# Optimization experiments

Measured on AMD Instinct MI355X. Metric: run time of the kernel, lower is better.

## Reference

```python
import jax, jax.numpy as jnp
import numpy as np

NS, NI, NC, C, E, M = 50000, 20000, 1000, 128, 1000000, 250000


def setup_inputs() -> dict:
    key = jax.random.key(0)
    ks = jax.random.split(key, 12)
    xavier = (2.0 / (C + C)) ** 0.5  # xavier_normal_ std for square weight
    return {
        "stu_x": jax.random.normal(ks[0], (NS, C), jnp.float32),
        "item_x": jax.random.normal(ks[1], (NI, C), jnp.float32),
        "conc_x": jax.random.normal(ks[2], (NC, C), jnp.float32),
        "W_stu": jax.random.normal(ks[3], (C, C), jnp.float32) * xavier,
        "b_stu": jnp.zeros((C,), jnp.float32),
        "W_item": jax.random.normal(ks[4], (C, C), jnp.float32) * xavier,
        "b_item": jnp.zeros((C,), jnp.float32),
        "W_pred": jax.random.normal(ks[5], (1, C), jnp.float32) * ((2.0 / (1 + C)) ** 0.5),
        "b_pred": jnp.zeros((1,), jnp.float32),
        "stu_track": jax.random.randint(ks[6], (E,), 0, NS, jnp.int32),
        "item_index": jax.random.randint(ks[7], (E,), 0, NI, jnp.int32),
        "conc_index": jax.random.randint(ks[8], (E,), 0, NC, jnp.int32),
        "mean_index": jax.random.randint(ks[9], (E,), 0, M, jnp.int32),
        "num_segments": M,
    }


def _segment_mean(vals, seg_ids, num_segments):
    sums = jax.ops.segment_sum(vals, seg_ids, num_segments=num_segments)
    cnt = jax.ops.segment_sum(jnp.ones((vals.shape[0], 1), vals.dtype), seg_ids,
                              num_segments=num_segments)
    return sums / jnp.maximum(cnt, 1.0)


def reference(stu_x, item_x, conc_x, W_stu, b_stu, W_item, b_item, W_pred, b_pred,
              stu_track, item_index, conc_index, mean_index, num_segments):
    # Feature (stu): shared lin_l=lin_r; aggregate is identity -> per-edge output
    conc_s = conc_x @ W_stu.T          # [NC, C] projected source (concepts)
    stu_p = stu_x @ W_stu.T            # [NS, C] projected target (students)
    stu_feature = jax.nn.sigmoid(conc_s[conc_index] + stu_p[stu_track] + b_stu)  # [E, C]

    # Feature (item): SparseTensor(row=item, col=conc) -> x_j from conc, x_i from item
    conc_i = conc_x @ W_item.T         # [NC, C]
    item_p = item_x @ W_item.T         # [NI, C]
    item_feature = jax.nn.sigmoid(conc_i[conc_index] + item_p[item_index] + b_item)  # [E, C]

    # scatter-mean of per-edge difference over mean_index groups
    pred_input = _segment_mean(stu_feature - item_feature, mean_index, num_segments)  # [M, C]
    pred = jax.nn.sigmoid(pred_input @ W_pred.T + b_pred)  # [M, 1]
    return pred.reshape(-1)
```

## Files before the change

### kernel.cpp

```cpp
#include <hip/hip_runtime.h>

typedef unsigned short u16;
typedef unsigned int   u32;

typedef short short8 __attribute__((ext_vector_type(8)));
typedef float floatx4 __attribute__((ext_vector_type(4)));

#define CDIM 128
#define K_NEG_LOG2E -1.4426950408889634f
#define CNT_SCALE 16777216.0

__device__ __forceinline__ float bf2f_lo(u32 h) {
    union { u32 u; float f; } v; v.u = h << 16; return v.f;
}
__device__ __forceinline__ float bf2f_hi(u32 h) {
    union { u32 u; float f; } v; v.u = h & 0xffff0000u; return v.f;
}
__device__ __forceinline__ u16 f2bf(float f) {
    union { float f; u32 u; } v; v.f = f;
    u32 u = v.u;
    return (u16)((u + 0x7FFFu + ((u >> 16) & 1u)) >> 16);
}
__device__ __forceinline__ float sig_std(float x) {
    return __builtin_amdgcn_rcpf(1.0f + __builtin_amdgcn_exp2f(x * K_NEG_LOG2E));
}

__device__ __forceinline__ float rowsum16(float v) {
    int x;
    x = __builtin_amdgcn_update_dpp(0, __float_as_int(v), 0x111, 0xF, 0xF, true);
    v += __int_as_float(x);
    x = __builtin_amdgcn_update_dpp(0, __float_as_int(v), 0x112, 0xF, 0xF, true);
    v += __int_as_float(x);
    x = __builtin_amdgcn_update_dpp(0, __float_as_int(v), 0x114, 0xF, 0xF, true);
    v += __int_as_float(x);
    x = __builtin_amdgcn_update_dpp(0, __float_as_int(v), 0x118, 0xF, 0xF, true);
    v += __int_as_float(x);
    return v;
}

__global__ __launch_bounds__(256) void prep_kernel(
    const float* __restrict__ Wstu, const float* __restrict__ Witem,
    u32* __restrict__ Wbf_pair, float4* __restrict__ zero4, int nZero4,
    const int* __restrict__ stu_track, const int* __restrict__ item_index,
    const int* __restrict__ conc_index, const int* __restrict__ mean_index,
    int4* __restrict__ idx4, int E)
{
    const int tid = blockIdx.x * blockDim.x + threadIdx.x;
    const int stride = gridDim.x * blockDim.x;
    for (int i = tid; i < 16384; i += stride) {
        const float* W = (i & 8192) ? (Witem - 16384) : Wstu;
        const int j = i * 2;
        u32 lo = f2bf(W[j]     * K_NEG_LOG2E);
        u32 hi = f2bf(W[j + 1] * K_NEG_LOG2E);
        Wbf_pair[i] = lo | (hi << 16);
    }
    const float4 z = {0.f, 0.f, 0.f, 0.f};
    for (int i = tid; i < nZero4; i += stride) zero4[i] = z;
    for (int e = tid; e < E; e += stride) {
        int4 t;
        t.x = stu_track[e]  << 8;
        t.y = item_index[e] << 8;
        t.z = conc_index[e] << 9;
        t.w = mean_index[e] << 3;
        idx4[e] = t;
    }
}

__device__ __forceinline__ void proj_tile16(
    const float* __restrict__ X, const u16* __restrict__ Wbf,
    const float* __restrict__ bias, u16* __restrict__ out,
    int nrows, int ostride, int ooff, int row0, int lane)
{
    const int m = lane & 15;
    const int g = lane >> 4;

    short8 a[4];
    {
        int arow = row0 + m;
        if (arow >= nrows) arow = nrows - 1;
        const float* xrow = X + (size_t)arow * CDIM;
#pragma unroll
        for (int s = 0; s < 4; ++s) {
            float4 f0 = *(const float4*)(xrow + s * 32 + g * 8);
            float4 f1 = *(const float4*)(xrow + s * 32 + g * 8 + 4);
            a[s][0] = (short)f2bf(f0.x); a[s][1] = (short)f2bf(f0.y);
            a[s][2] = (short)f2bf(f0.z); a[s][3] = (short)f2bf(f0.w);
            a[s][4] = (short)f2bf(f1.x); a[s][5] = (short)f2bf(f1.y);
            a[s][6] = (short)f2bf(f1.z); a[s][7] = (short)f2bf(f1.w);
        }
    }

#pragma unroll
    for (int ct = 0; ct < 8; ++ct) {
        const u16* wrow = Wbf + (size_t)(ct * 16 + m) * CDIM;
        floatx4 acc = {0.f, 0.f, 0.f, 0.f};
#pragma unroll
        for (int s = 0; s < 4; ++s) {
            short8 b = *(const short8*)(wrow + s * 32 + g * 8);
            acc = __builtin_amdgcn_mfma_f32_16x16x32_bf16(a[s], b, acc, 0, 0, 0);
        }
        const int col = ct * 16 + m;
        const float badd = bias ? bias[col] * K_NEG_LOG2E : 0.f;
#pragma unroll
        for (int i = 0; i < 4; ++i) {
            int r = row0 + g * 4 + i;
            if (r < nrows)
                out[(size_t)r * ostride + ooff + col] =
                    f2bf(__builtin_amdgcn_exp2f(acc[i] + badd));
        }
    }
}

__global__ __launch_bounds__(256) void proj4_kernel(
    const float* __restrict__ stu_x, const float* __restrict__ item_x,
    const float* __restrict__ conc_x,
    const u16* __restrict__ Wstu_bf, const u16* __restrict__ Witem_bf,
    const float* __restrict__ b_stu, const float* __restrict__ b_item,
    u16* __restrict__ stu_p, u16* __restrict__ item_p, u16* __restrict__ conc_cat,
    int NS, int NI, int NC)
{
    const int lane = threadIdx.x & 63;
    int w = blockIdx.x * 4 + (threadIdx.x >> 6);
    const int T0 = (NS + 15) / 16, T1 = (NI + 15) / 16, T2 = (NC + 15) / 16;

    if (w < T0) { proj_tile16(stu_x, Wstu_bf, nullptr, stu_p, NS, 128, 0, w * 16, lane); return; }
    w -= T0;
    if (w < T1) { proj_tile16(item_x, Witem_bf, nullptr, item_p, NI, 128, 0, w * 16, lane); return; }
    w -= T1;
    if (w < T2) { proj_tile16(conc_x, Wstu_bf, b_stu, conc_cat, NC, 256, 0, w * 16, lane); return; }
    w -= T2;
    if (w < T2) { proj_tile16(conc_x, Witem_bf, b_item, conc_cat, NC, 256, 128, w * 16, lane); return; }
}

__global__ __launch_bounds__(256) void edge_kernel(
    const u16* __restrict__ stu_p, const u16* __restrict__ item_p,
    const u16* __restrict__ conc_cat,
    const int4* __restrict__ idx4,
    const float* __restrict__ w_pred,
    double* __restrict__ sc, int E)
{
    const int lane = threadIdx.x & 63;
    const int sub  = lane & 15;
    const int g    = lane >> 4;
    const int waveId = (int)((blockIdx.x * blockDim.x + threadIdx.x) >> 6);
    const int S      = (int)((gridDim.x * blockDim.x) >> 6);

    const float4 wA = ((const float4*)w_pred)[sub * 2];
    const float4 wB = ((const float4*)w_pred)[sub * 2 + 1];
    float2 w2[4];
    w2[0] = make_float2(wA.x, wA.y); w2[1] = make_float2(wA.z, wA.w);
    w2[2] = make_float2(wB.x, wB.y); w2[3] = make_float2(wB.z, wB.w);
    const u32 lane_off = (u32)sub * 16;

    const int nQuads = (E + 3) >> 2;
    int q = waveId;
    if (q >= nQuads) return;

    auto ldidx = [&](int qq) -> int4 {
        int e = qq * 4 + g;
        e = (e < E) ? e : (E - 1);
        return idx4[e];
    };
    auto compute = [&](const uint4& sv, const uint4& iv,
                       const uint4& ca, const uint4& cb,
                       const int4& I, int qq) {
        const u32 su[4] = {sv.x, sv.y, sv.z, sv.w};
        const u32 iu[4] = {iv.x, iv.y, iv.z, iv.w};
        const u32 au[4] = {ca.x, ca.y, ca.z, ca.w};
        const u32 bu[4] = {cb.x, cb.y, cb.z, cb.w};
        float2 vacc = make_float2(0.f, 0.f);
#pragma unroll
        for (int j = 0; j < 4; ++j) {
            float2 A  = make_float2(bf2f_lo(au[j]), bf2f_hi(au[j]));
            float2 Sx = make_float2(bf2f_lo(su[j]), bf2f_hi(su[j]));
            float2 B  = make_float2(bf2f_lo(bu[j]), bf2f_hi(bu[j]));
            float2 Ix = make_float2(bf2f_lo(iu[j]), bf2f_hi(iu[j]));
            float2 ea = A * Sx;
            float2 eb = B * Ix;
            float2 u  = make_float2(eb.x + 1.f, eb.y + 1.f);
            float2 den = make_float2(fmaf(ea.x, u.x, u.x),
                                     fmaf(ea.y, u.y, u.y));
            float2 num = eb - ea;
            float2 rd = make_float2(__builtin_amdgcn_rcpf(den.x),
                                    __builtin_amdgcn_rcpf(den.y));
            float2 t  = make_float2(num.x * rd.x, num.y * rd.y);
            vacc.x = fmaf(t.x, w2[j].x, vacc.x);
            vacc.y = fmaf(t.y, w2[j].y, vacc.y);
        }
        float v = rowsum16(vacc.x + vacc.y);
        if (sub == 15 && (qq * 4 + g) < E)
            atomicAdd((double*)((char*)sc + (u32)I.w), (double)v + CNT_SCALE);
    };

#define GATH(I_, sv_, iv_, ca_, cb_) { \
        sv_ = *(const uint4*)((const char*)stu_p  + ((u32)(I_).x + lane_off)); \
        iv_ = *(const uint4*)((const char*)item_p + ((u32)(I_).y + lane_off)); \
        const char* cp_ = (const char*)conc_cat + ((u32)(I_).z + lane_off); \
        ca_ = *(const uint4*)cp_; cb_ = *(const uint4*)(cp_ + 256); }

#define STEP(DA, DB, IA, IB, IC) { \
        GATH(I##IB, sv##DB, iv##DB, ca##DB, cb##DB); \
        I##IC = ldidx(q + 2 * S); \
        __builtin_amdgcn_sched_barrier(0); \
        compute(sv##DA, iv##DA, ca##DA, cb##DA, I##IA, q); \
        q += S; \
        if (q >= nQuads) break; }

    int4 I0 = ldidx(q), I1 = ldidx(q + S), I2, I3;
    uint4 sv0, iv0, ca0, cb0, sv1, iv1, ca1, cb1;
    GATH(I0, sv0, iv0, ca0, cb0);

    for (;;) {
        STEP(0, 1, 0, 1, 2)
        STEP(1, 0, 1, 2, 3)
        STEP(0, 1, 2, 3, 0)
        STEP(1, 0, 3, 0, 1)
    }
#undef STEP
#undef GATH
}

__global__ __launch_bounds__(256) void final_kernel(
    const double* __restrict__ sc,
    const float* __restrict__ b_pred, float* __restrict__ out, int M)
{
    const int i = blockIdx.x * blockDim.x + threadIdx.x;
    if (i < M) {
        const double acc = sc[i];
        const double cnt = rint(acc * (1.0 / CNT_SCALE));
        const double sum = acc - cnt * CNT_SCALE;
        const float mean = (float)(sum / fmax(cnt, 1.0));
        out[i] = sig_std(mean + b_pred[0]);
    }
}

extern "C" void kernel_launch(void* const* d_in, const int* in_sizes, int n_in,
                              void* d_out, int out_size, void* d_ws, size_t ws_size,
                              hipStream_t stream) {
    const float* stu_x    = (const float*)d_in[0];
    const float* item_x   = (const float*)d_in[1];
    const float* conc_x   = (const float*)d_in[2];
    const float* W_stu    = (const float*)d_in[3];
    const float* b_stu    = (const float*)d_in[4];
    const float* W_item   = (const float*)d_in[5];
    const float* b_item   = (const float*)d_in[6];
    const float* W_pred   = (const float*)d_in[7];
    const float* b_pred   = (const float*)d_in[8];
    const int* stu_track  = (const int*)d_in[9];
    const int* item_index = (const int*)d_in[10];
    const int* conc_index = (const int*)d_in[11];
    const int* mean_index = (const int*)d_in[12];

    const int NS = in_sizes[0] / CDIM;
    const int NI = in_sizes[1] / CDIM;
    const int NC = in_sizes[2] / CDIM;
    const int E  = in_sizes[9];
    const int M  = out_size;

    double* sc     = (double*)d_ws;
    u16* Wstu_bf   = (u16*)(sc + M);
    u16* Witem_bf  = Wstu_bf + CDIM * CDIM;
    u16* stu_p     = Witem_bf + CDIM * CDIM;
    u16* item_p    = stu_p  + (size_t)NS * CDIM;
    u16* conc_cat  = item_p + (size_t)NI * CDIM;
    int4* idx4     = (int4*)(conc_cat + (size_t)NC * 256);

    const int nZero4 = (int)(((size_t)M * sizeof(double)) / 16);
    prep_kernel<<<1024, 256, 0, stream>>>(W_stu, W_item, (u32*)Wstu_bf,
                                          (float4*)sc, nZero4,
                                          stu_track, item_index, conc_index,
                                          mean_index, idx4, E);

    const int T0 = (NS + 15) / 16, T1 = (NI + 15) / 16, T2 = (NC + 15) / 16;
    const int totalWaves = T0 + T1 + 2 * T2;
    proj4_kernel<<<(totalWaves + 3) / 4, 256, 0, stream>>>(
        stu_x, item_x, conc_x, Wstu_bf, Witem_bf, b_stu, b_item,
        stu_p, item_p, conc_cat, NS, NI, NC);

    edge_kernel<<<4096, 256, 0, stream>>>(stu_p, item_p, conc_cat,
                                          idx4, W_pred, sc, E);

    final_kernel<<<(M + 255) / 256, 256, 0, stream>>>(sc, b_pred, (float*)d_out, M);
}
```

Before: 201.2 us.

## Fuse prep and projection kernels, stage bf16 weights in LDS per block

Merges the prep kernel (weight conversion, zeroing, index packing) and the projection kernel into one launch. Each projection block converts its weight matrix to bf16 into padded LDS, and extra blocks do the zeroing and index packing. This removes a launch and a global round trip for the weights, at the cost of redundant weight conversion in every block. The edge kernel's per-edge math is also reformulated and the DPP row reduction is replaced with xor shuffles, which may be slower than DPP.

```diff
diff --git a/kernel.cpp b/kernel.cpp
--- a/kernel.cpp
+++ b/kernel.cpp
@@ -9,6 +9,9 @@
 #define CDIM 128
 #define K_NEG_LOG2E -1.4426950408889634f
 #define CNT_SCALE 16777216.0
+
+#define WLDS_STRIDE 136
+#define PACK_BLOCKS 512
 
 __device__ __forceinline__ float bf2f_lo(u32 h) {
     union { u32 u; float f; } v; v.u = h << 16; return v.f;
@@ -25,49 +28,8 @@
     return __builtin_amdgcn_rcpf(1.0f + __builtin_amdgcn_exp2f(x * K_NEG_LOG2E));
 }
 
-__device__ __forceinline__ float rowsum16(float v) {
-    int x;
-    x = __builtin_amdgcn_update_dpp(0, __float_as_int(v), 0x111, 0xF, 0xF, true);
-    v += __int_as_float(x);
-    x = __builtin_amdgcn_update_dpp(0, __float_as_int(v), 0x112, 0xF, 0xF, true);
-    v += __int_as_float(x);
-    x = __builtin_amdgcn_update_dpp(0, __float_as_int(v), 0x114, 0xF, 0xF, true);
-    v += __int_as_float(x);
-    x = __builtin_amdgcn_update_dpp(0, __float_as_int(v), 0x118, 0xF, 0xF, true);
-    v += __int_as_float(x);
-    return v;
-}
-
-__global__ __launch_bounds__(256) void prep_kernel(
-    const float* __restrict__ Wstu, const float* __restrict__ Witem,
-    u32* __restrict__ Wbf_pair, float4* __restrict__ zero4, int nZero4,
-    const int* __restrict__ stu_track, const int* __restrict__ item_index,
-    const int* __restrict__ conc_index, const int* __restrict__ mean_index,
-    int4* __restrict__ idx4, int E)
-{
-    const int tid = blockIdx.x * blockDim.x + threadIdx.x;
-    const int stride = gridDim.x * blockDim.x;
-    for (int i = tid; i < 16384; i += stride) {
-        const float* W = (i & 8192) ? (Witem - 16384) : Wstu;
-        const int j = i * 2;
-        u32 lo = f2bf(W[j]     * K_NEG_LOG2E);
-        u32 hi = f2bf(W[j + 1] * K_NEG_LOG2E);
-        Wbf_pair[i] = lo | (hi << 16);
-    }
-    const float4 z = {0.f, 0.f, 0.f, 0.f};
-    for (int i = tid; i < nZero4; i += stride) zero4[i] = z;
-    for (int e = tid; e < E; e += stride) {
-        int4 t;
-        t.x = stu_track[e]  << 8;
-        t.y = item_index[e] << 8;
-        t.z = conc_index[e] << 9;
-        t.w = mean_index[e] << 3;
-        idx4[e] = t;
-    }
-}
-
-__device__ __forceinline__ void proj_tile16(
-    const float* __restrict__ X, const u16* __restrict__ Wbf,
+__device__ __forceinline__ void proj_tile16_lds(
+    const float* __restrict__ X, const u16* __restrict__ wlds,
     const float* __restrict__ bias, u16* __restrict__ out,
     int nrows, int ostride, int ooff, int row0, int lane)
 {
@@ -92,7 +54,7 @@
 
 #pragma unroll
     for (int ct = 0; ct < 8; ++ct) {
-        const u16* wrow = Wbf + (size_t)(ct * 16 + m) * CDIM;
+        const u16* wrow = wlds + (size_t)(ct * 16 + m) * WLDS_STRIDE;
         floatx4 acc = {0.f, 0.f, 0.f, 0.f};
 #pragma unroll
         for (int s = 0; s < 4; ++s) {
@@ -111,25 +73,75 @@
     }
 }
 
-__global__ __launch_bounds__(256) void proj4_kernel(
+__global__ __launch_bounds__(256) void fused_prep_proj(
     const float* __restrict__ stu_x, const float* __restrict__ item_x,
     const float* __restrict__ conc_x,
-    const u16* __restrict__ Wstu_bf, const u16* __restrict__ Witem_bf,
+    const float* __restrict__ Wstu, const float* __restrict__ Witem,
     const float* __restrict__ b_stu, const float* __restrict__ b_item,
     u16* __restrict__ stu_p, u16* __restrict__ item_p, u16* __restrict__ conc_cat,
+    float4* __restrict__ zero4, int nZero4,
+    const int* __restrict__ stu_track, const int* __restrict__ item_index,
+    const int* __restrict__ conc_index, const int* __restrict__ mean_index,
+    int4* __restrict__ idx4, int E,
     int NS, int NI, int NC)
 {
+    __shared__ u16 wlds[128 * WLDS_STRIDE];
+
+    const int PB0 = (NS + 63) / 64, PB1 = (NI + 63) / 64, PB2 = (NC + 63) / 64;
+    const int PBtot = PB0 + PB1 + 2 * PB2;
+    int b = blockIdx.x;
+
+    if (b >= PBtot) {
+        const int tid = (b - PBtot) * 256 + threadIdx.x;
+        const int stride = PACK_BLOCKS * 256;
+        const float4 z = {0.f, 0.f, 0.f, 0.f};
+        for (int i = tid; i < nZero4; i += stride) zero4[i] = z;
+        for (int e = tid; e < E; e += stride) {
+            int4 t;
+            t.x = stu_track[e]  << 8;
+            t.y = item_index[e] << 8;
+            t.z = conc_index[e] << 9;
+            t.w = mean_index[e] << 3;
+            idx4[e] = t;
+        }
+        return;
+    }
+
+    const float* X; const float* Wsel; const float* bias;
+    u16* out; int nrows, ostride, ooff, base;
+    if (b < PB0)      { X = stu_x;  Wsel = Wstu;  bias = nullptr; out = stu_p;
+                        nrows = NS; ostride = 128; ooff = 0;   base = b * 64; }
+    else if ((b -= PB0) < PB1)
+                      { X = item_x; Wsel = Witem; bias = nullptr; out = item_p;
+                        nrows = NI; ostride = 128; ooff = 0;   base = b * 64; }
+    else if ((b -= PB1) < PB2)
+                      { X = conc_x; Wsel = Wstu;  bias = b_stu;  out = conc_cat;
+                        nrows = NC; ostride = 256; ooff = 0;   base = b * 64; }
+    else              { b -= PB2;
+                        X = conc_x; Wsel = Witem; bias = b_item; out = conc_cat;
+                        nrows = NC; ostride = 256; ooff = 128; base = b * 64; }
+
+    {
+        const int t   = threadIdx.x;
+        const int col = t >> 1;
+        const int k0  = (t & 1) * 64;
+        const float4* src = (const float4*)(Wsel + col * 128 + k0);
+        u32* dst = (u32*)(wlds + col * WLDS_STRIDE + k0);
+#pragma unroll
+        for (int i = 0; i < 16; ++i) {
+            float4 f = src[i];
+            dst[2 * i]     = (u32)f2bf(f.x * K_NEG_LOG2E) |
+                             ((u32)f2bf(f.y * K_NEG_LOG2E) << 16);
+            dst[2 * i + 1] = (u32)f2bf(f.z * K_NEG_LOG2E) |
+                             ((u32)f2bf(f.w * K_NEG_LOG2E) << 16);
+        }
+    }
+    __syncthreads();
+
     const int lane = threadIdx.x & 63;
-    int w = blockIdx.x * 4 + (threadIdx.x >> 6);
-    const int T0 = (NS + 15) / 16, T1 = (NI + 15) / 16, T2 = (NC + 15) / 16;
-
-    if (w < T0) { proj_tile16(stu_x, Wstu_bf, nullptr, stu_p, NS, 128, 0, w * 16, lane); return; }
-    w -= T0;
-    if (w < T1) { proj_tile16(item_x, Witem_bf, nullptr, item_p, NI, 128, 0, w * 16, lane); return; }
-    w -= T1;
-    if (w < T2) { proj_tile16(conc_x, Wstu_bf, b_stu, conc_cat, NC, 256, 0, w * 16, lane); return; }
-    w -= T2;
-    if (w < T2) { proj_tile16(conc_x, Witem_bf, b_item, conc_cat, NC, 256, 128, w * 16, lane); return; }
+    const int row0 = base + (threadIdx.x >> 6) * 16;
+    if (row0 < nrows)
+        proj_tile16_lds(X, wlds, bias, out, nrows, ostride, ooff, row0, lane);
 }
 
 __global__ __launch_bounds__(256) void edge_kernel(
@@ -168,6 +180,7 @@
         const u32 iu[4] = {iv.x, iv.y, iv.z, iv.w};
         const u32 au[4] = {ca.x, ca.y, ca.z, ca.w};
         const u32 bu[4] = {cb.x, cb.y, cb.z, cb.w};
+        const float2 one = make_float2(1.f, 1.f);
         float2 vacc = make_float2(0.f, 0.f);
 #pragma unroll
         for (int j = 0; j < 4; ++j) {
@@ -177,18 +190,18 @@
             float2 Ix = make_float2(bf2f_lo(iu[j]), bf2f_hi(iu[j]));
             float2 ea = A * Sx;
             float2 eb = B * Ix;
-            float2 u  = make_float2(eb.x + 1.f, eb.y + 1.f);
-            float2 den = make_float2(fmaf(ea.x, u.x, u.x),
-                                     fmaf(ea.y, u.y, u.y));
+            float2 den = (ea + one) * (eb + one);
             float2 num = eb - ea;
             float2 rd = make_float2(__builtin_amdgcn_rcpf(den.x),
                                     __builtin_amdgcn_rcpf(den.y));
-            float2 t  = make_float2(num.x * rd.x, num.y * rd.y);
-            vacc.x = fmaf(t.x, w2[j].x, vacc.x);
-            vacc.y = fmaf(t.y, w2[j].y, vacc.y);
-        }
-        float v = rowsum16(vacc.x + vacc.y);
-        if (sub == 15 && (qq * 4 + g) < E)
+            vacc += (num * rd) * w2[j];
+        }
+        float v = vacc.x + vacc.y;
+        v += __shfl_xor(v, 1, 64);
+        v += __shfl_xor(v, 2, 64);
+        v += __shfl_xor(v, 4, 64);
+        v += __shfl_xor(v, 8, 64);
+        if (sub == 0 && (qq * 4 + g) < E)
             atomicAdd((double*)((char*)sc + (u32)I.w), (double)v + CNT_SCALE);
     };
 
@@ -258,24 +271,21 @@
     const int M  = out_size;
 
     double* sc     = (double*)d_ws;
-    u16* Wstu_bf   = (u16*)(sc + M);
-    u16* Witem_bf  = Wstu_bf + CDIM * CDIM;
-    u16* stu_p     = Witem_bf + CDIM * CDIM;
+    u16* stu_p     = (u16*)(sc + M);
     u16* item_p    = stu_p  + (size_t)NS * CDIM;
     u16* conc_cat  = item_p + (size_t)NI * CDIM;
     int4* idx4     = (int4*)(conc_cat + (size_t)NC * 256);
 
     const int nZero4 = (int)(((size_t)M * sizeof(double)) / 16);
-    prep_kernel<<<1024, 256, 0, stream>>>(W_stu, W_item, (u32*)Wstu_bf,
-                                          (float4*)sc, nZero4,
-                                          stu_track, item_index, conc_index,
-                                          mean_index, idx4, E);
-
-    const int T0 = (NS + 15) / 16, T1 = (NI + 15) / 16, T2 = (NC + 15) / 16;
-    const int totalWaves = T0 + T1 + 2 * T2;
-    proj4_kernel<<<(totalWaves + 3) / 4, 256, 0, stream>>>(
-        stu_x, item_x, conc_x, Wstu_bf, Witem_bf, b_stu, b_item,
-        stu_p, item_p, conc_cat, NS, NI, NC);
+    const int PB0 = (NS + 63) / 64, PB1 = (NI + 63) / 64, PB2 = (NC + 63) / 64;
+    const int PBtot = PB0 + PB1 + 2 * PB2;
+
+    fused_prep_proj<<<PBtot + PACK_BLOCKS, 256, 0, stream>>>(
+        stu_x, item_x, conc_x, W_stu, W_item, b_stu, b_item,
+        stu_p, item_p, conc_cat,
+        (float4*)sc, nZero4,
+        stu_track, item_index, conc_index, mean_index, idx4, E,
+        NS, NI, NC);
 
     edge_kernel<<<4096, 256, 0, stream>>>(stu_p, item_p, conc_cat,
                                           idx4, W_pred, sc, E);
```

After: 196.0 us. -2.6%, faster.
